# Performance work log

Hardware: AMD Instinct MI355X
Metric: run time of the kernel (lower is better)

## Reference

```python
import jax, jax.numpy as jnp
import numpy as np

N = 100000   # nodes
E = 1000000  # edges
D = 128      # hidden dim (all n_hidden entries)
ED = 21      # edge_dim hard-coded in the module


def setup_inputs() -> dict:
    key = jax.random.key(0)
    ks = jax.random.split(key, 32)
    w = lambda k, shape: (jax.random.normal(k, shape, dtype=jnp.float32) * 0.05)
    inp = {
        "G": jax.random.normal(ks[0], (N, D), dtype=jnp.float32),
        "edge_index": jax.random.randint(ks[1], (2, E), 0, N),
        "edge_attribute": jax.random.normal(ks[2], (E, ED), dtype=jnp.float32),
        # 3-layer node embedding MLP (stacked since all dims are D)
        "emb_W": w(ks[3], (3, D, D)), "emb_b": w(ks[4], (3, D)),
        # 2 ResGatedGraphConv layers (conv3 is unused in forward)
        "key_W": w(ks[5], (2, D, D)), "key_b": w(ks[6], (2, D)),
        "qry_W": w(ks[7], (2, D, D)), "qry_b": w(ks[8], (2, D)),
        "val_W": w(ks[9], (2, D, D)), "val_b": w(ks[10], (2, D)),
        "skp_W": w(ks[11], (2, D, D)), "skp_b": w(ks[12], (2, D)),
        "edg_W": w(ks[13], (2, ED, D)), "edg_b": w(ks[14], (2, D)),
        # graph linears
        "g1_W": w(ks[15], (D, D)), "g1_b": w(ks[16], (D,)),
        "g2_W": w(ks[17], (D, D)), "g2_b": w(ks[18], (D,)),
        # head: concat(node, graph_mean) -> 2D -> D -> D -> 1
        "h1_W": w(ks[19], (2 * D, D)), "h1_b": w(ks[20], (D,)),
        "h2_W": w(ks[21], (D, D)), "h2_b": w(ks[22], (D,)),
        "h3_W": w(ks[23], (D, 1)), "h3_b": w(ks[24], (1,)),
    }
    return inp


def reference(G, edge_index, edge_attribute,
              emb_W, emb_b, key_W, key_b, qry_W, qry_b, val_W, val_b,
              skp_W, skp_b, edg_W, edg_b,
              g1_W, g1_b, g2_W, g2_b, h1_W, h1_b, h2_W, h2_b, h3_W, h3_b):
    x = G
    # embedding MLP: Linear -> ReLU x3
    for i in range(3):
        x = jax.nn.relu(x @ emb_W[i] + emb_b[i])
    src, dst = edge_index[0], edge_index[1]
    # ResGatedGraphConv (PyG): out_i = W_skip x_i + sum_j sigmoid(k_i + q_j + W_e e_ij) * v_j
    for i in range(2):
        k = x @ key_W[i] + key_b[i]   # per target node i
        q = x @ qry_W[i] + qry_b[i]   # per source node j
        v = x @ val_W[i] + val_b[i]
        eta = jax.nn.sigmoid(k[dst] + q[src] + edge_attribute @ edg_W[i] + edg_b[i])  # [E, D]
        agg = jax.ops.segment_sum(eta * v[src], dst, num_segments=N)  # scatter-add [N, D]
        x = jax.nn.relu(agg + x @ skp_W[i] + skp_b[i])
    x = jax.nn.relu(x @ g1_W + g1_b)
    x = x @ g2_W + g2_b
    # per-node concat with mean-pooled graph embedding (vectorized form of the Python loop)
    gmean = jnp.mean(x, axis=0)
    u = jnp.concatenate([x, jnp.broadcast_to(gmean, x.shape)], axis=-1)  # [N, 2D]
    u = jax.nn.relu(u @ h1_W + h1_b)
    u = jax.nn.relu(u @ h2_W + h2_b)
    return u @ h3_W + h3_b  # [N, 1]
```

## Files before the change

### kernel.cpp

```cpp
#include <hip/hip_runtime.h>
#include <hip/hip_bf16.h>

#define DD 128
#define LW 136

typedef __attribute__((ext_vector_type(8))) short bf16x8;
typedef __attribute__((ext_vector_type(4))) float f32x4;

__device__ __forceinline__ void cvt8(const float4 a0, const float4 a1,
                                     bf16x8& hi, bf16x8& lo)
{
    float af[8] = {a0.x, a0.y, a0.z, a0.w, a1.x, a1.y, a1.z, a1.w};
    union { unsigned int u[4]; bf16x8 v; } H, L;
    #pragma unroll
    for (int i = 0; i < 4; ++i) {
        unsigned int b0 = __float_as_uint(af[2*i]);
        unsigned int b1 = __float_as_uint(af[2*i+1]);
        unsigned int h0 = b0 & 0xFFFF0000u;
        unsigned int h1 = b1 & 0xFFFF0000u;
        H.u[i] = (h0 >> 16) | h1;
        float r0 = af[2*i]   - __uint_as_float(h0);
        float r1 = af[2*i+1] - __uint_as_float(h1);
        L.u[i] = (__float_as_uint(r0) >> 16) | (__float_as_uint(r1) & 0xFFFF0000u);
    }
    hi = H.v; lo = L.v;
}

__device__ __forceinline__ float fsig(float z)
{
    return __builtin_amdgcn_rcpf(1.f + __expf(-z));
}

__device__ __forceinline__ void mfma_step(
    const unsigned short* __restrict__ WH, const unsigned short* __restrict__ WL,
    int wavecol, int l15, int kb,
    const bf16x8 ah[4], const bf16x8 al[4], f32x4 acc[4][2])
{
    bf16x8 bh[2], bl[2];
    #pragma unroll
    for (int ni = 0; ni < 2; ++ni) {
        int m = wavecol + ni * 16 + l15;
        bh[ni] = *(const bf16x8*)(WH + (size_t)m * DD + kb);
        bl[ni] = *(const bf16x8*)(WL + (size_t)m * DD + kb);
    }
    #pragma unroll
    for (int mi = 0; mi < 4; ++mi)
        #pragma unroll
        for (int ni = 0; ni < 2; ++ni) {
            acc[mi][ni] = __builtin_amdgcn_mfma_f32_16x16x32_bf16(ah[mi], bh[ni], acc[mi][ni], 0, 0, 0);
            acc[mi][ni] = __builtin_amdgcn_mfma_f32_16x16x32_bf16(ah[mi], bl[ni], acc[mi][ni], 0, 0, 0);
            acc[mi][ni] = __builtin_amdgcn_mfma_f32_16x16x32_bf16(al[mi], bh[ni], acc[mi][ni], 0, 0, 0);
        }
}

__device__ __forceinline__ void glb_layer(
    const float* __restrict__ X, int ldX, const int arow[4],
    const unsigned short* __restrict__ WU,
    int wavecol, int l15, int kg, f32x4 acc[4][2])
{
    const unsigned short* WH = WU;
    const unsigned short* WL = WU + 16384;
    #pragma unroll
    for (int kc = 0; kc < 4; ++kc) {
        const int kb = kc * 32 + kg;
        bf16x8 ah[4], al[4];
        #pragma unroll
        for (int mi = 0; mi < 4; ++mi) {
            const float* p = X + (size_t)arow[mi] * ldX + kb;
            float4 a0 = *(const float4*)p;
            float4 a1 = *(const float4*)(p + 4);
            cvt8(a0, a1, ah[mi], al[mi]);
        }
        mfma_step(WH, WL, wavecol, l15, kb, ah, al, acc);
    }
}

__device__ __forceinline__ void lds_layer(
    const unsigned short (*AH)[LW], const unsigned short (*AL)[LW],
    const unsigned short* __restrict__ WU,
    int wavecol, int l15, int kg, f32x4 acc[4][2])
{
    const unsigned short* WH = WU;
    const unsigned short* WL = WU + 16384;
    #pragma unroll
    for (int kc = 0; kc < 4; ++kc) {
        const int kb = kc * 32 + kg;
        bf16x8 ah[4], al[4];
        #pragma unroll
        for (int mi = 0; mi < 4; ++mi) {
            ah[mi] = *(const bf16x8*)&AH[mi * 16 + l15][kb];
            al[mi] = *(const bf16x8*)&AL[mi * 16 + l15][kb];
        }
        mfma_step(WH, WL, wavecol, l15, kb, ah, al, acc);
    }
}

__device__ __forceinline__ void epi_lds(
    const f32x4 acc[4][2], unsigned short (*AH)[LW], unsigned short (*AL)[LW],
    const float* __restrict__ bias, int wavecol, int l15, int rg, int relu)
{
    #pragma unroll
    for (int ni = 0; ni < 2; ++ni) {
        const int col = wavecol + ni * 16 + l15;
        const float bv = bias[col];
        #pragma unroll
        for (int mi = 0; mi < 4; ++mi)
            #pragma unroll
            for (int r = 0; r < 4; ++r) {
                const int row = mi * 16 + rg + r;
                float v = acc[mi][ni][r] + bv;
                if (relu) v = fmaxf(v, 0.f);
                unsigned int u = __float_as_uint(v), h = u & 0xFFFF0000u;
                float res = v - __uint_as_float(h);
                AH[row][col] = (unsigned short)(h >> 16);
                AL[row][col] = (unsigned short)(__float_as_uint(res) >> 16);
            }
    }
}

__global__ __launch_bounds__(256) void fused_emb3q(
    const float* __restrict__ G, const unsigned short* __restrict__ Wt,
    const float* __restrict__ embb, const float* __restrict__ biasCat,
    float* __restrict__ bfused, int N)
{
    __shared__ unsigned short AH[64][LW], AL[64][LW];
    const int lane = threadIdx.x & 63, wid = threadIdx.x >> 6;
    const int wavecol = wid * 32;
    const int l15 = lane & 15, kg = (lane >> 4) * 8, rg = (lane >> 4) * 4;
    const int row0 = blockIdx.x * 64;

    int arow[4];
    #pragma unroll
    for (int mi = 0; mi < 4; ++mi) {
        int r = row0 + mi * 16 + l15;
        arow[mi] = r < N ? r : N - 1;
    }

    f32x4 acc[4][2] = {};
    glb_layer(G, DD, arow, Wt, wavecol, l15, kg, acc);
    epi_lds(acc, AH, AL, embb, wavecol, l15, rg, 1);
    __syncthreads();

    #pragma unroll
    for (int mi = 0; mi < 4; ++mi)
        #pragma unroll
        for (int ni = 0; ni < 2; ++ni) acc[mi][ni] = (f32x4){0,0,0,0};
    lds_layer(AH, AL, Wt + 32768, wavecol, l15, kg, acc);
    __syncthreads();
    epi_lds(acc, AH, AL, embb + 128, wavecol, l15, rg, 1);
    __syncthreads();

    #pragma unroll
    for (int mi = 0; mi < 4; ++mi)
        #pragma unroll
        for (int ni = 0; ni < 2; ++ni) acc[mi][ni] = (f32x4){0,0,0,0};
    lds_layer(AH, AL, Wt + 65536, wavecol, l15, kg, acc);
    __syncthreads();
    epi_lds(acc, AH, AL, embb + 256, wavecol, l15, rg, 1);
    __syncthreads();

    for (int cb = 0; cb < 4; ++cb) {
        #pragma unroll
        for (int mi = 0; mi < 4; ++mi)
            #pragma unroll
            for (int ni = 0; ni < 2; ++ni) acc[mi][ni] = (f32x4){0,0,0,0};
        lds_layer(AH, AL, Wt + (size_t)(3 + cb) * 32768, wavecol, l15, kg, acc);
        #pragma unroll
        for (int ni = 0; ni < 2; ++ni) {
            const int gcol = cb * 128 + wavecol + ni * 16 + l15;
            const float bv = biasCat[gcol];
            #pragma unroll
            for (int mi = 0; mi < 4; ++mi)
                #pragma unroll
                for (int r = 0; r < 4; ++r) {
                    int row = row0 + mi * 16 + rg + r;
                    if (row < N)
                        bfused[(size_t)row * 512 + gcol] = acc[mi][ni][r] + bv;
                }
        }
    }
}

__global__ __launch_bounds__(256) void fused_kqvs(
    float* __restrict__ bfused, const unsigned short* __restrict__ Wt,
    const float* __restrict__ biasCat, int N)
{
    __shared__ unsigned short AH[64][LW], AL[64][LW];
    const int tid = threadIdx.x;
    const int lane = tid & 63, wid = tid >> 6;
    const int wavecol = wid * 32;
    const int l15 = lane & 15, kg = (lane >> 4) * 8, rg = (lane >> 4) * 4;
    const int row0 = blockIdx.x * 64;

    for (int idx = tid; idx < 64 * 128; idx += 256) {
        const int row = idx >> 7, col = idx & 127;
        int gr = row0 + row; if (gr >= N) gr = N - 1;
        float v = bfused[(size_t)gr * 512 + col];
        unsigned int u = __float_as_uint(v), h = u & 0xFFFF0000u;
        float res = v - __uint_as_float(h);
        AH[row][col] = (unsigned short)(h >> 16);
        AL[row][col] = (unsigned short)(__float_as_uint(res) >> 16);
    }
    __syncthreads();

    f32x4 acc[4][2];
    for (int cb = 0; cb < 4; ++cb) {
        #pragma unroll
        for (int mi = 0; mi < 4; ++mi)
            #pragma unroll
            for (int ni = 0; ni < 2; ++ni) acc[mi][ni] = (f32x4){0,0,0,0};
        lds_layer(AH, AL, Wt + (size_t)cb * 32768, wavecol, l15, kg, acc);
        #pragma unroll
        for (int ni = 0; ni < 2; ++ni) {
            const int gcol = cb * 128 + wavecol + ni * 16 + l15;
            const float bv = biasCat[cb * 128 + wavecol + ni * 16 + l15 - cb * 128 + cb * 128];
            #pragma unroll
            for (int mi = 0; mi < 4; ++mi)
                #pragma unroll
                for (int r = 0; r < 4; ++r) {
                    int row = row0 + mi * 16 + rg + r;
                    if (row < N)
                        bfused[(size_t)row * 512 + gcol] = acc[mi][ni][r] + bv;
                }
        }
    }
}

__global__ __launch_bounds__(256) void fused_g12(
    float* __restrict__ bfused, const unsigned short* __restrict__ Wt,
    const float* __restrict__ g1b, const float* __restrict__ g2b,
    float* __restrict__ gsum, int N)
{
    __shared__ unsigned short AH[64][LW], AL[64][LW];
    __shared__ float csum[128];
    const int tid = threadIdx.x;
    const int lane = tid & 63, wid = tid >> 6;
    const int wavecol = wid * 32;
    const int l15 = lane & 15, kg = (lane >> 4) * 8, rg = (lane >> 4) * 4;
    const int row0 = blockIdx.x * 64;

    if (tid < 128) csum[tid] = 0.f;

    int arow[4];
    #pragma unroll
    for (int mi = 0; mi < 4; ++mi) {
        int r = row0 + mi * 16 + l15;
        arow[mi] = r < N ? r : N - 1;
    }

    f32x4 acc[4][2] = {};
    glb_layer(bfused, 512, arow, Wt, wavecol, l15, kg, acc);
    epi_lds(acc, AH, AL, g1b, wavecol, l15, rg, 1);
    __syncthreads();

    #pragma unroll
    for (int mi = 0; mi < 4; ++mi)
        #pragma unroll
        for (int ni = 0; ni < 2; ++ni) acc[mi][ni] = (f32x4){0,0,0,0};
    lds_layer(AH, AL, Wt + 32768, wavecol, l15, kg, acc);

    #pragma unroll
    for (int ni = 0; ni < 2; ++ni) {
        const int col = wavecol + ni * 16 + l15;
        const float bv = g2b[col];
        float part = 0.f;
        #pragma unroll
        for (int mi = 0; mi < 4; ++mi)
            #pragma unroll
            for (int r = 0; r < 4; ++r) {
                int row = row0 + mi * 16 + rg + r;
                if (row < N) {
                    float v = acc[mi][ni][r] + bv;
                    bfused[(size_t)row * 512 + 128 + col] = v;
                    part += v;
                }
            }
        atomicAdd(&csum[col], part);
    }
    __syncthreads();
    if (tid < 128) atomicAdd(&gsum[tid], csum[tid]);
}

__global__ __launch_bounds__(256) void fused_head(
    const float* __restrict__ bfused, const unsigned short* __restrict__ Wt,
    const float* __restrict__ cvec, const float* __restrict__ h2b,
    const float* __restrict__ h3w, const float* __restrict__ h3b,
    float* __restrict__ out, int N)
{
    __shared__ unsigned short AH[64][LW], AL[64][LW];
    const int tid = threadIdx.x;
    const int lane = tid & 63, wid = tid >> 6;
    const int wavecol = wid * 32;
    const int l15 = lane & 15, kg = (lane >> 4) * 8, rg = (lane >> 4) * 4;
    const int row0 = blockIdx.x * 64;

    int arow[4];
    #pragma unroll
    for (int mi = 0; mi < 4; ++mi) {
        int r = row0 + mi * 16 + l15;
        arow[mi] = r < N ? r : N - 1;
    }

    f32x4 acc[4][2] = {};
    glb_layer(bfused + 128, 512, arow, Wt, wavecol, l15, kg, acc);
    epi_lds(acc, AH, AL, cvec, wavecol, l15, rg, 1);
    __syncthreads();

    #pragma unroll
    for (int mi = 0; mi < 4; ++mi)
        #pragma unroll
        for (int ni = 0; ni < 2; ++ni) acc[mi][ni] = (f32x4){0,0,0,0};
    lds_layer(AH, AL, Wt + 32768, wavecol, l15, kg, acc);
    __syncthreads();
    epi_lds(acc, AH, AL, h2b, wavecol, l15, rg, 1);
    __syncthreads();

    const int row = tid >> 2, seg = tid & 3;
    float s = 0.f;
    #pragma unroll 8
    for (int j = 0; j < 32; ++j) {
        int col = seg * 32 + j;
        float xv = __uint_as_float((unsigned int)AH[row][col] << 16)
                 + __uint_as_float((unsigned int)AL[row][col] << 16);
        s = fmaf(xv, h3w[col], s);
    }
    s += __shfl_xor(s, 1, 64);
    s += __shfl_xor(s, 2, 64);
    if (seg == 0 && row0 + row < N) out[row0 + row] = s + h3b[0];
}

__global__ __launch_bounds__(256) void prep_weights(
    const float* __restrict__ embW, const float* __restrict__ keyW,
    const float* __restrict__ qryW, const float* __restrict__ valW,
    const float* __restrict__ skpW, const float* __restrict__ g1W,
    const float* __restrict__ g2W, const float* __restrict__ h1W,
    const float* __restrict__ h2W,
    const float* __restrict__ keyb, const float* __restrict__ qryb,
    const float* __restrict__ valb, const float* __restrict__ skpb,
    unsigned short* __restrict__ Wt, float* __restrict__ biasCat)
{
    const int u = blockIdx.x;
    const int t = threadIdx.x;
    __shared__ float T[128][129];

    const float* src;
    if (u < 3)       src = embW + (size_t)u * 16384;
    else if (u < 7)  { const float* p[4] = {keyW, qryW, valW, skpW}; src = p[u - 3]; }
    else if (u < 11) { const float* p[4] = {keyW, qryW, valW, skpW}; src = p[u - 7] + 16384; }
    else if (u == 11) src = g1W;
    else if (u == 12) src = g2W;
    else if (u == 13) src = h1W;
    else              src = h2W;

    #pragma unroll
    for (int i = 0; i < 64; ++i) {
        int idx = t + 256 * i;
        T[idx >> 7][idx & 127] = src[idx];
    }
    __syncthreads();

    unsigned short* dH = Wt + (size_t)u * 32768;
    unsigned short* dL = dH + 16384;
    const int m = t >> 1, kbase = (t & 1) * 64;
    for (int j = 0; j < 64; ++j) {
        int k = kbase + j;
        float a = T[k][m];
        unsigned int b = __float_as_uint(a);
        unsigned int h = b & 0xFFFF0000u;
        float r = a - __uint_as_float(h);
        dH[m * 128 + k] = (unsigned short)(h >> 16);
        dL[m * 128 + k] = (unsigned short)(__float_as_uint(r) >> 16);
    }

    if (u == 0) {
        for (int x = t; x < 1024; x += 256) {
            int L = x >> 9, c = x & 511;
            const float* bp = (c < 128) ? keyb : (c < 256) ? qryb : (c < 384) ? valb : skpb;
            biasCat[x] = bp[L * 128 + (c & 127)];
        }
    }
}

__global__ void hist_kernel(const int* __restrict__ dstA, int* __restrict__ hist, int E)
{
    for (int e = blockIdx.x * blockDim.x + threadIdx.x; e < E;
         e += gridDim.x * blockDim.x)
        atomicAdd(&hist[dstA[e]], 1);
}

__global__ __launch_bounds__(256) void scan1_kernel(
    const int* __restrict__ in, int n_in,
    int* __restrict__ out, int* __restrict__ bsum, int n)
{
    __shared__ int wtot[4];
    const int t = threadIdx.x, lane = t & 63, wv = t >> 6;
    const int base = blockIdx.x * 1024 + t * 4;
    int v[4]; int sum = 0;
    #pragma unroll
    for (int j = 0; j < 4; ++j) {
        int idx = base + j;
        v[j] = (idx < n_in) ? in[idx] : 0;
        sum += v[j];
    }
    int incl = sum;
    #pragma unroll
    for (int d = 1; d < 64; d <<= 1) {
        int y = __shfl_up(incl, d, 64);
        if (lane >= d) incl += y;
    }
    if (lane == 63) wtot[wv] = incl;
    __syncthreads();
    int woff = 0;
    for (int w = 0; w < wv; ++w) woff += wtot[w];
    int run = woff + incl - sum;
    #pragma unroll
    for (int j = 0; j < 4; ++j) {
        int idx = base + j;
        if (idx < n) out[idx] = run;
        run += v[j];
    }
    if (t == 0)
        bsum[blockIdx.x] = wtot[0] + wtot[1] + wtot[2] + wtot[3];
}

__global__ void scan2_kernel(int* __restrict__ bsum, int nb)
{
    if (blockIdx.x == 0 && threadIdx.x == 0) {
        int run = 0;
        for (int i = 0; i < nb; ++i) { int t = bsum[i]; bsum[i] = run; run += t; }
    }
}

__global__ __launch_bounds__(256) void scan3_kernel(
    int* __restrict__ out, const int* __restrict__ bsum,
    int* __restrict__ cursor, int n, int n_nodes)
{
    const int base = blockIdx.x * 1024 + threadIdx.x * 4;
    const int add = bsum[blockIdx.x];
    #pragma unroll
    for (int j = 0; j < 4; ++j) {
        int idx = base + j;
        if (idx < n) {
            int vv = out[idx] + add;
            out[idx] = vv;
            if (idx < n_nodes) cursor[idx] = vv;
        }
    }
}

__global__ void scatter_kernel(const int* __restrict__ srcA, const int* __restrict__ dstA,
                               int* __restrict__ cursor, int* __restrict__ perm,
                               int* __restrict__ srcp, int E)
{
    for (int e = blockIdx.x * blockDim.x + threadIdx.x; e < E;
         e += gridDim.x * blockDim.x) {
        int d = dstA[e];
        int pos = atomicAdd(&cursor[d], 1);
        perm[pos] = e;
        srcp[pos] = srcA[e];
    }
}

__global__ void permute_ea_kernel(const float* __restrict__ ea, const int* __restrict__ perm,
                                  float* __restrict__ eaP, long E)
{
    const long total = E * 24;
    for (long t = (long)blockIdx.x * blockDim.x + threadIdx.x; t < total;
         t += (long)gridDim.x * blockDim.x) {
        long i = t / 24; int j = (int)(t - i * 24);
        eaP[t] = (j < 21) ? ea[(size_t)perm[i] * 21 + j] : 0.f;
    }
}

__global__ __launch_bounds__(256) void edge_agg13(
    const int* __restrict__ row_ptr, const int* __restrict__ srcp,
    const float* __restrict__ eaP,
    const float* __restrict__ We, const float* __restrict__ be,
    float* __restrict__ fused, int N)
{
    const int wv = threadIdx.x >> 6, lane = threadIdx.x & 63;
    const int d = blockIdx.x * 4 + wv;
    if (d >= N) return;
    const int c = lane * 2;

    float2 w[21];
    #pragma unroll
    for (int j = 0; j < 21; ++j)
        w[j] = *(const float2*)(We + j * DD + c);
    const float2 b2 = *(const float2*)(be + c);
    const float2 kd = *(const float2*)(fused + (size_t)d * 512 + c);
    const float2 sk = *(const float2*)(fused + (size_t)d * 512 + 384 + c);

    float ax = 0.f, ay = 0.f;
    const int i0 = __builtin_amdgcn_readfirstlane(row_ptr[d]);
    const int i1 = __builtin_amdgcn_readfirstlane(row_ptr[d + 1]);

    for (int i = i0; i < i1; i += 2) {
        const int iA = i;
        const int iB = (i + 1 < i1) ? i + 1 : i1 - 1;
        const float wgtB = (i + 1 < i1) ? 1.f : 0.f;

        const int sA = __builtin_amdgcn_readfirstlane(srcp[iA]);
        const int sB = __builtin_amdgcn_readfirstlane(srcp[iB]);

        const float* eA = eaP + (size_t)iA * 24;
        const float* eB = eaP + (size_t)iB * 24;
        float aA[21], aB[21];
        #pragma unroll
        for (int j = 0; j < 21; ++j) { aA[j] = eA[j]; aB[j] = eB[j]; }

        const float* fpA = fused + (size_t)sA * 512;
        const float* fpB = fused + (size_t)sB * 512;
        float2 qA = *(const float2*)(fpA + 128 + c);
        float2 vA = *(const float2*)(fpA + 256 + c);
        float2 qB = *(const float2*)(fpB + 128 + c);
        float2 vB = *(const float2*)(fpB + 256 + c);

        float pxA[4] = {0,0,0,0}, pyA[4] = {0,0,0,0};
        float pxB[4] = {0,0,0,0}, pyB[4] = {0,0,0,0};
        #pragma unroll
        for (int j = 0; j < 21; ++j) {
            int s = j & 3;
            pxA[s] = fmaf(aA[j], w[j].x, pxA[s]);
            pyA[s] = fmaf(aA[j], w[j].y, pyA[s]);
            pxB[s] = fmaf(aB[j], w[j].x, pxB[s]);
            pyB[s] = fmaf(aB[j], w[j].y, pyB[s]);
        }
        float exA = (pxA[0] + pxA[1]) + (pxA[2] + pxA[3]) + b2.x;
        float eyA = (pyA[0] + pyA[1]) + (pyA[2] + pyA[3]) + b2.y;
        float exB = (pxB[0] + pxB[1]) + (pxB[2] + pxB[3]) + b2.x;
        float eyB = (pyB[0] + pyB[1]) + (pyB[2] + pyB[3]) + b2.y;

        float gxA = fsig(kd.x + qA.x + exA);
        float gyA = fsig(kd.y + qA.y + eyA);
        float gxB = wgtB * fsig(kd.x + qB.x + exB);
        float gyB = wgtB * fsig(kd.y + qB.y + eyB);

        ax = fmaf(gxA, vA.x, ax);
        ay = fmaf(gyA, vA.y, ay);
        ax = fmaf(gxB, vB.x, ax);
        ay = fmaf(gyB, vB.y, ay);
    }

    float* xr = fused + (size_t)d * 512;
    xr[c]     = fmaxf(ax + sk.x, 0.f);
    xr[c + 1] = fmaxf(ay + sk.y, 0.f);
}

__global__ void cvec_kernel(const float* __restrict__ gsum, const float* __restrict__ h1W,
                            const float* __restrict__ h1b, float* __restrict__ cvec, float invN)
{
    const int m = threadIdx.x;
    float acc = h1b[m];
    for (int k = 0; k < 128; ++k)
        acc = fmaf(gsum[k] * invN, h1W[(size_t)(128 + k) * DD + m], acc);
    cvec[m] = acc;
}

extern "C" void kernel_launch(void* const* d_in, const int* in_sizes, int n_in,
                              void* d_out, int out_size, void* d_ws, size_t ws_size,
                              hipStream_t stream)
{
    const float* G    = (const float*)d_in[0];
    const int*   ei   = (const int*)  d_in[1];
    const float* ea   = (const float*)d_in[2];
    const float* embW = (const float*)d_in[3];
    const float* embb = (const float*)d_in[4];
    const float* keyW = (const float*)d_in[5];
    const float* keyb = (const float*)d_in[6];
    const float* qryW = (const float*)d_in[7];
    const float* qryb = (const float*)d_in[8];
    const float* valW = (const float*)d_in[9];
    const float* valb = (const float*)d_in[10];
    const float* skpW = (const float*)d_in[11];
    const float* skpb = (const float*)d_in[12];
    const float* edgW = (const float*)d_in[13];
    const float* edgb = (const float*)d_in[14];
    const float* g1W  = (const float*)d_in[15];
    const float* g1b  = (const float*)d_in[16];
    const float* g2W  = (const float*)d_in[17];
    const float* g2b  = (const float*)d_in[18];
    const float* h1W  = (const float*)d_in[19];
    const float* h1b  = (const float*)d_in[20];
    const float* h2W  = (const float*)d_in[21];
    const float* h2b  = (const float*)d_in[22];
    const float* h3W  = (const float*)d_in[23];
    const float* h3b  = (const float*)d_in[24];

    const int N = in_sizes[0] / DD;
    const int E = in_sizes[2] / 21;
    const int* srcA = ei;
    const int* dstA = ei + E;

    float* bfused = (float*)d_ws;
    float* gsum   = bfused + (size_t)N * 512;
    float* cvec   = gsum + DD;
    float* biasCat= cvec + DD;
    unsigned short* Wt = (unsigned short*)(biasCat + 1024);
    int* hist = (int*)((char*)Wt + (size_t)15 * 32768 * 2);
    int* row  = hist + N;
    int* cur  = row + N + 1;
    int* bsum = cur + N;
    int* perm = bsum + 128;
    int* srcp = perm + E;
    float* eaP = (float*)(srcp + E);

    const int fgrid   = (N + 63) / 64;
    const int aggGrid = (N + 3) / 4;
    const int nScan = N + 1;
    const int nb = (nScan + 1023) / 1024;

    prep_weights<<<15, 256, 0, stream>>>(embW, keyW, qryW, valW, skpW,
                                         g1W, g2W, h1W, h2W,
                                         keyb, qryb, valb, skpb, Wt, biasCat);
    hipMemsetAsync(hist, 0, (size_t)N * sizeof(int), stream);
    hipMemsetAsync(gsum, 0, DD * sizeof(float), stream);
    hist_kernel<<<1024, 256, 0, stream>>>(dstA, hist, E);
    scan1_kernel<<<nb, 256, 0, stream>>>(hist, N, row, bsum, nScan);
    scan2_kernel<<<1, 64, 0, stream>>>(bsum, nb);
    scan3_kernel<<<nb, 256, 0, stream>>>(row, bsum, cur, nScan, N);
    scatter_kernel<<<1024, 256, 0, stream>>>(srcA, dstA, cur, perm, srcp, E);
    permute_ea_kernel<<<2048, 256, 0, stream>>>(ea, perm, eaP, (long)E);

    #define UNIT(u) (Wt + (size_t)(u) * 32768)

    fused_emb3q<<<fgrid, 256, 0, stream>>>(G, Wt, embb, biasCat, bfused, N);

    edge_agg13<<<aggGrid, 256, 0, stream>>>(row, srcp, eaP,
                                            edgW + 0, edgb + 0, bfused, N);

    fused_kqvs<<<fgrid, 256, 0, stream>>>(bfused, UNIT(7), biasCat + 512, N);
    edge_agg13<<<aggGrid, 256, 0, stream>>>(row, srcp, eaP,
                                            edgW + 21*DD, edgb + DD, bfused, N);

    fused_g12<<<fgrid, 256, 0, stream>>>(bfused, UNIT(11), g1b, g2b, gsum, N);

    cvec_kernel<<<1, DD, 0, stream>>>(gsum, h1W, h1b, cvec, 1.0f / (float)N);

    fused_head<<<fgrid, 256, 0, stream>>>(bfused, UNIT(13), cvec, h2b, h3W, h3b,
                                          (float*)d_out, N);
}
```

Before: 1.093 ms.

## Fuse edge-attribute permutation into scatter and prefetch next gather in edge aggregation

The CSR scatter kernel now copies each edge's 21 attributes directly into the permuted padded buffer, which removes the separate perm array and the permute_ea kernel. The edge aggregation kernel software-pipelines the q/v gathers by loading the next pair of source rows while the current pair is computed. The intent is to cut one pass over the edge attributes and hide gather latency. In exchange, the scatter writes are strided per thread (less coalesced) and the loop uses more registers. The pad columns of eaP are no longer zeroed, but they are never read.

```diff
diff --git a/kernel.cpp b/kernel.cpp
--- a/kernel.cpp
+++ b/kernel.cpp
@@ -213,7 +213,7 @@
         #pragma unroll
         for (int ni = 0; ni < 2; ++ni) {
             const int gcol = cb * 128 + wavecol + ni * 16 + l15;
-            const float bv = biasCat[cb * 128 + wavecol + ni * 16 + l15 - cb * 128 + cb * 128];
+            const float bv = biasCat[gcol];
             #pragma unroll
             for (int mi = 0; mi < 4; ++mi)
                 #pragma unroll
@@ -448,31 +448,23 @@
     }
 }
 
-__global__ void scatter_kernel(const int* __restrict__ srcA, const int* __restrict__ dstA,
-                               int* __restrict__ cursor, int* __restrict__ perm,
-                               int* __restrict__ srcp, int E)
+__global__ void scatter_ea(const int* __restrict__ srcA, const int* __restrict__ dstA,
+                           const float* __restrict__ ea, int* __restrict__ cursor,
+                           int* __restrict__ srcp, float* __restrict__ eaP, int E)
 {
     for (int e = blockIdx.x * blockDim.x + threadIdx.x; e < E;
          e += gridDim.x * blockDim.x) {
         int d = dstA[e];
         int pos = atomicAdd(&cursor[d], 1);
-        perm[pos] = e;
         srcp[pos] = srcA[e];
-    }
-}
-
-__global__ void permute_ea_kernel(const float* __restrict__ ea, const int* __restrict__ perm,
-                                  float* __restrict__ eaP, long E)
-{
-    const long total = E * 24;
-    for (long t = (long)blockIdx.x * blockDim.x + threadIdx.x; t < total;
-         t += (long)gridDim.x * blockDim.x) {
-        long i = t / 24; int j = (int)(t - i * 24);
-        eaP[t] = (j < 21) ? ea[(size_t)perm[i] * 21 + j] : 0.f;
-    }
-}
-
-__global__ __launch_bounds__(256) void edge_agg13(
+        const float* s = ea + (size_t)e * 21;
+        float* q = eaP + (size_t)pos * 24;
+        #pragma unroll
+        for (int j = 0; j < 21; ++j) q[j] = s[j];
+    }
+}
+
+__global__ __launch_bounds__(256) void edge_agg14(
     const int* __restrict__ row_ptr, const int* __restrict__ srcp,
     const float* __restrict__ eaP,
     const float* __restrict__ We, const float* __restrict__ be,
@@ -495,26 +487,43 @@
     const int i0 = __builtin_amdgcn_readfirstlane(row_ptr[d]);
     const int i1 = __builtin_amdgcn_readfirstlane(row_ptr[d + 1]);
 
-    for (int i = i0; i < i1; i += 2) {
-        const int iA = i;
-        const int iB = (i + 1 < i1) ? i + 1 : i1 - 1;
-        const float wgtB = (i + 1 < i1) ? 1.f : 0.f;
-
-        const int sA = __builtin_amdgcn_readfirstlane(srcp[iA]);
-        const int sB = __builtin_amdgcn_readfirstlane(srcp[iB]);
-
-        const float* eA = eaP + (size_t)iA * 24;
-        const float* eB = eaP + (size_t)iB * 24;
-        float aA[21], aB[21];
-        #pragma unroll
-        for (int j = 0; j < 21; ++j) { aA[j] = eA[j]; aB[j] = eB[j]; }
-
+    float2 qA = {0,0}, vA = {0,0}, qB = {0,0}, vB = {0,0};
+    if (i0 < i1) {
+        const int iB0 = (i0 + 1 < i1) ? i0 + 1 : i0;
+        const int sA = __builtin_amdgcn_readfirstlane(srcp[i0]);
+        const int sB = __builtin_amdgcn_readfirstlane(srcp[iB0]);
         const float* fpA = fused + (size_t)sA * 512;
         const float* fpB = fused + (size_t)sB * 512;
-        float2 qA = *(const float2*)(fpA + 128 + c);
-        float2 vA = *(const float2*)(fpA + 256 + c);
-        float2 qB = *(const float2*)(fpB + 128 + c);
-        float2 vB = *(const float2*)(fpB + 256 + c);
+        qA = *(const float2*)(fpA + 128 + c);
+        vA = *(const float2*)(fpA + 256 + c);
+        qB = *(const float2*)(fpB + 128 + c);
+        vB = *(const float2*)(fpB + 256 + c);
+    }
+
+    for (int i = i0; i < i1; i += 2) {
+        const float wgtB = (i + 1 < i1) ? 1.f : 0.f;
+        const int iBc = (i + 1 < i1) ? i + 1 : i;
+
+        const float2 cqA = qA, cvA = vA, cqB = qB, cvB = vB;
+
+        const int inx = i + 2;
+        if (inx < i1) {
+            const int inB = (inx + 1 < i1) ? inx + 1 : inx;
+            const int sA = __builtin_amdgcn_readfirstlane(srcp[inx]);
+            const int sB = __builtin_amdgcn_readfirstlane(srcp[inB]);
+            const float* fpA = fused + (size_t)sA * 512;
+            const float* fpB = fused + (size_t)sB * 512;
+            qA = *(const float2*)(fpA + 128 + c);
+            vA = *(const float2*)(fpA + 256 + c);
+            qB = *(const float2*)(fpB + 128 + c);
+            vB = *(const float2*)(fpB + 256 + c);
+        }
+
+        const float* eA = eaP + (size_t)i * 24;
+        const float* eB = eaP + (size_t)iBc * 24;
+        float aA[21], aB[21];
+        #pragma unroll
+        for (int j = 0; j < 21; ++j) { aA[j] = eA[j]; aB[j] = eB[j]; }
 
         float pxA[4] = {0,0,0,0}, pyA[4] = {0,0,0,0};
         float pxB[4] = {0,0,0,0}, pyB[4] = {0,0,0,0};
@@ -531,15 +540,15 @@
         float exB = (pxB[0] + pxB[1]) + (pxB[2] + pxB[3]) + b2.x;
         float eyB = (pyB[0] + pyB[1]) + (pyB[2] + pyB[3]) + b2.y;
 
-        float gxA = fsig(kd.x + qA.x + exA);
-        float gyA = fsig(kd.y + qA.y + eyA);
-        float gxB = wgtB * fsig(kd.x + qB.x + exB);
-        float gyB = wgtB * fsig(kd.y + qB.y + eyB);
-
-        ax = fmaf(gxA, vA.x, ax);
-        ay = fmaf(gyA, vA.y, ay);
-        ax = fmaf(gxB, vB.x, ax);
-        ay = fmaf(gyB, vB.y, ay);
+        float gxA = fsig(kd.x + cqA.x + exA);
+        float gyA = fsig(kd.y + cqA.y + eyA);
+        float gxB = wgtB * fsig(kd.x + cqB.x + exB);
+        float gyB = wgtB * fsig(kd.y + cqB.y + eyB);
+
+        ax = fmaf(gxA, cvA.x, ax);
+        ay = fmaf(gyA, cvA.y, ay);
+        ax = fmaf(gxB, cvB.x, ax);
+        ay = fmaf(gyB, cvB.y, ay);
     }
 
     float* xr = fused + (size_t)d * 512;
@@ -601,8 +610,7 @@
     int* row  = hist + N;
     int* cur  = row + N + 1;
     int* bsum = cur + N;
-    int* perm = bsum + 128;
-    int* srcp = perm + E;
+    int* srcp = bsum + 128;
     float* eaP = (float*)(srcp + E);
 
     const int fgrid   = (N + 63) / 64;
@@ -619,18 +627,17 @@
     scan1_kernel<<<nb, 256, 0, stream>>>(hist, N, row, bsum, nScan);
     scan2_kernel<<<1, 64, 0, stream>>>(bsum, nb);
     scan3_kernel<<<nb, 256, 0, stream>>>(row, bsum, cur, nScan, N);
-    scatter_kernel<<<1024, 256, 0, stream>>>(srcA, dstA, cur, perm, srcp, E);
-    permute_ea_kernel<<<2048, 256, 0, stream>>>(ea, perm, eaP, (long)E);
+    scatter_ea<<<1024, 256, 0, stream>>>(srcA, dstA, ea, cur, srcp, eaP, E);
 
     #define UNIT(u) (Wt + (size_t)(u) * 32768)
 
     fused_emb3q<<<fgrid, 256, 0, stream>>>(G, Wt, embb, biasCat, bfused, N);
 
-    edge_agg13<<<aggGrid, 256, 0, stream>>>(row, srcp, eaP,
+    edge_agg14<<<aggGrid, 256, 0, stream>>>(row, srcp, eaP,
                                             edgW + 0, edgb + 0, bfused, N);
 
     fused_kqvs<<<fgrid, 256, 0, stream>>>(bfused, UNIT(7), biasCat + 512, N);
-    edge_agg13<<<aggGrid, 256, 0, stream>>>(row, srcp, eaP,
+    edge_agg14<<<aggGrid, 256, 0, stream>>>(row, srcp, eaP,
                                             edgW + 21*DD, edgb + DD, bfused, N);
 
     fused_g12<<<fgrid, 256, 0, stream>>>(bfused, UNIT(11), g1b, g2b, gsum, N);
```

Result: faster. 1.028 ms (median of 2 runs) (-5.9%).

## Fuse edge-attribute permutation into CSR scatter and persist edge aggregation grid

Applied to the files above, without the earlier changes.

The CSR scatter kernel now copies each edge's 21 attributes straight to their sorted slot. This removes the separate perm array and the permute_ea pass with its per-element index divide. The edge aggregation kernel becomes a grid-stride loop over destination nodes with a fixed 2048-block grid, so the 21 edge weights are loaded once per wave instead of once per node. The trade-offs are fewer waves to hide gather latency, uncoalesced 21-float writes in the scatter, and the 3 padding floats in eaP no longer being written (they are unread).

```diff
diff --git a/kernel.cpp b/kernel.cpp
--- a/kernel.cpp
+++ b/kernel.cpp
@@ -213,7 +213,7 @@
         #pragma unroll
         for (int ni = 0; ni < 2; ++ni) {
             const int gcol = cb * 128 + wavecol + ni * 16 + l15;
-            const float bv = biasCat[cb * 128 + wavecol + ni * 16 + l15 - cb * 128 + cb * 128];
+            const float bv = biasCat[gcol];
             #pragma unroll
             for (int mi = 0; mi < 4; ++mi)
                 #pragma unroll
@@ -448,39 +448,29 @@
     }
 }
 
-__global__ void scatter_kernel(const int* __restrict__ srcA, const int* __restrict__ dstA,
-                               int* __restrict__ cursor, int* __restrict__ perm,
-                               int* __restrict__ srcp, int E)
+__global__ void scatter_ea(const int* __restrict__ srcA, const int* __restrict__ dstA,
+                           const float* __restrict__ ea, int* __restrict__ cursor,
+                           int* __restrict__ srcp, float* __restrict__ eaP, int E)
 {
     for (int e = blockIdx.x * blockDim.x + threadIdx.x; e < E;
          e += gridDim.x * blockDim.x) {
         int d = dstA[e];
         int pos = atomicAdd(&cursor[d], 1);
-        perm[pos] = e;
         srcp[pos] = srcA[e];
-    }
-}
-
-__global__ void permute_ea_kernel(const float* __restrict__ ea, const int* __restrict__ perm,
-                                  float* __restrict__ eaP, long E)
-{
-    const long total = E * 24;
-    for (long t = (long)blockIdx.x * blockDim.x + threadIdx.x; t < total;
-         t += (long)gridDim.x * blockDim.x) {
-        long i = t / 24; int j = (int)(t - i * 24);
-        eaP[t] = (j < 21) ? ea[(size_t)perm[i] * 21 + j] : 0.f;
-    }
-}
-
-__global__ __launch_bounds__(256) void edge_agg13(
+        const float* s = ea + (size_t)e * 21;
+        float* q = eaP + (size_t)pos * 24;
+        #pragma unroll
+        for (int j = 0; j < 21; ++j) q[j] = s[j];
+    }
+}
+
+__global__ __launch_bounds__(256) void edge_agg16(
     const int* __restrict__ row_ptr, const int* __restrict__ srcp,
     const float* __restrict__ eaP,
     const float* __restrict__ We, const float* __restrict__ be,
     float* __restrict__ fused, int N)
 {
     const int wv = threadIdx.x >> 6, lane = threadIdx.x & 63;
-    const int d = blockIdx.x * 4 + wv;
-    if (d >= N) return;
     const int c = lane * 2;
 
     float2 w[21];
@@ -488,63 +478,68 @@
     for (int j = 0; j < 21; ++j)
         w[j] = *(const float2*)(We + j * DD + c);
     const float2 b2 = *(const float2*)(be + c);
-    const float2 kd = *(const float2*)(fused + (size_t)d * 512 + c);
-    const float2 sk = *(const float2*)(fused + (size_t)d * 512 + 384 + c);
-
-    float ax = 0.f, ay = 0.f;
-    const int i0 = __builtin_amdgcn_readfirstlane(row_ptr[d]);
-    const int i1 = __builtin_amdgcn_readfirstlane(row_ptr[d + 1]);
-
-    for (int i = i0; i < i1; i += 2) {
-        const int iA = i;
-        const int iB = (i + 1 < i1) ? i + 1 : i1 - 1;
-        const float wgtB = (i + 1 < i1) ? 1.f : 0.f;
-
-        const int sA = __builtin_amdgcn_readfirstlane(srcp[iA]);
-        const int sB = __builtin_amdgcn_readfirstlane(srcp[iB]);
-
-        const float* eA = eaP + (size_t)iA * 24;
-        const float* eB = eaP + (size_t)iB * 24;
-        float aA[21], aB[21];
-        #pragma unroll
-        for (int j = 0; j < 21; ++j) { aA[j] = eA[j]; aB[j] = eB[j]; }
-
-        const float* fpA = fused + (size_t)sA * 512;
-        const float* fpB = fused + (size_t)sB * 512;
-        float2 qA = *(const float2*)(fpA + 128 + c);
-        float2 vA = *(const float2*)(fpA + 256 + c);
-        float2 qB = *(const float2*)(fpB + 128 + c);
-        float2 vB = *(const float2*)(fpB + 256 + c);
-
-        float pxA[4] = {0,0,0,0}, pyA[4] = {0,0,0,0};
-        float pxB[4] = {0,0,0,0}, pyB[4] = {0,0,0,0};
-        #pragma unroll
-        for (int j = 0; j < 21; ++j) {
-            int s = j & 3;
-            pxA[s] = fmaf(aA[j], w[j].x, pxA[s]);
-            pyA[s] = fmaf(aA[j], w[j].y, pyA[s]);
-            pxB[s] = fmaf(aB[j], w[j].x, pxB[s]);
-            pyB[s] = fmaf(aB[j], w[j].y, pyB[s]);
-        }
-        float exA = (pxA[0] + pxA[1]) + (pxA[2] + pxA[3]) + b2.x;
-        float eyA = (pyA[0] + pyA[1]) + (pyA[2] + pyA[3]) + b2.y;
-        float exB = (pxB[0] + pxB[1]) + (pxB[2] + pxB[3]) + b2.x;
-        float eyB = (pyB[0] + pyB[1]) + (pyB[2] + pyB[3]) + b2.y;
-
-        float gxA = fsig(kd.x + qA.x + exA);
-        float gyA = fsig(kd.y + qA.y + eyA);
-        float gxB = wgtB * fsig(kd.x + qB.x + exB);
-        float gyB = wgtB * fsig(kd.y + qB.y + eyB);
-
-        ax = fmaf(gxA, vA.x, ax);
-        ay = fmaf(gyA, vA.y, ay);
-        ax = fmaf(gxB, vB.x, ax);
-        ay = fmaf(gyB, vB.y, ay);
-    }
-
-    float* xr = fused + (size_t)d * 512;
-    xr[c]     = fmaxf(ax + sk.x, 0.f);
-    xr[c + 1] = fmaxf(ay + sk.y, 0.f);
+
+    const int dstride = gridDim.x * 4;
+
+    for (int d = blockIdx.x * 4 + wv; d < N; d += dstride) {
+        const float2 kd = *(const float2*)(fused + (size_t)d * 512 + c);
+        const float2 sk = *(const float2*)(fused + (size_t)d * 512 + 384 + c);
+
+        float ax = 0.f, ay = 0.f;
+        const int i0 = __builtin_amdgcn_readfirstlane(row_ptr[d]);
+        const int i1 = __builtin_amdgcn_readfirstlane(row_ptr[d + 1]);
+
+        for (int i = i0; i < i1; i += 2) {
+            const int iA = i;
+            const int iB = (i + 1 < i1) ? i + 1 : i1 - 1;
+            const float wgtB = (i + 1 < i1) ? 1.f : 0.f;
+
+            const int sA = __builtin_amdgcn_readfirstlane(srcp[iA]);
+            const int sB = __builtin_amdgcn_readfirstlane(srcp[iB]);
+
+            const float* eA = eaP + (size_t)iA * 24;
+            const float* eB = eaP + (size_t)iB * 24;
+            float aA[21], aB[21];
+            #pragma unroll
+            for (int j = 0; j < 21; ++j) { aA[j] = eA[j]; aB[j] = eB[j]; }
+
+            const float* fpA = fused + (size_t)sA * 512;
+            const float* fpB = fused + (size_t)sB * 512;
+            float2 qA = *(const float2*)(fpA + 128 + c);
+            float2 vA = *(const float2*)(fpA + 256 + c);
+            float2 qB = *(const float2*)(fpB + 128 + c);
+            float2 vB = *(const float2*)(fpB + 256 + c);
+
+            float pxA[4] = {0,0,0,0}, pyA[4] = {0,0,0,0};
+            float pxB[4] = {0,0,0,0}, pyB[4] = {0,0,0,0};
+            #pragma unroll
+            for (int j = 0; j < 21; ++j) {
+                int s = j & 3;
+                pxA[s] = fmaf(aA[j], w[j].x, pxA[s]);
+                pyA[s] = fmaf(aA[j], w[j].y, pyA[s]);
+                pxB[s] = fmaf(aB[j], w[j].x, pxB[s]);
+                pyB[s] = fmaf(aB[j], w[j].y, pyB[s]);
+            }
+            float exA = (pxA[0] + pxA[1]) + (pxA[2] + pxA[3]) + b2.x;
+            float eyA = (pyA[0] + pyA[1]) + (pyA[2] + pyA[3]) + b2.y;
+            float exB = (pxB[0] + pxB[1]) + (pxB[2] + pxB[3]) + b2.x;
+            float eyB = (pyB[0] + pyB[1]) + (pyB[2] + pyB[3]) + b2.y;
+
+            float gxA = fsig(kd.x + qA.x + exA);
+            float gyA = fsig(kd.y + qA.y + eyA);
+            float gxB = wgtB * fsig(kd.x + qB.x + exB);
+            float gyB = wgtB * fsig(kd.y + qB.y + eyB);
+
+            ax = fmaf(gxA, vA.x, ax);
+            ay = fmaf(gyA, vA.y, ay);
+            ax = fmaf(gxB, vB.x, ax);
+            ay = fmaf(gyB, vB.y, ay);
+        }
+
+        float* xr = fused + (size_t)d * 512;
+        xr[c]     = fmaxf(ax + sk.x, 0.f);
+        xr[c + 1] = fmaxf(ay + sk.y, 0.f);
+    }
 }
 
 __global__ void cvec_kernel(const float* __restrict__ gsum, const float* __restrict__ h1W,
@@ -601,12 +596,11 @@
     int* row  = hist + N;
     int* cur  = row + N + 1;
     int* bsum = cur + N;
-    int* perm = bsum + 128;
-    int* srcp = perm + E;
+    int* srcp = bsum + 128;
     float* eaP = (float*)(srcp + E);
 
     const int fgrid   = (N + 63) / 64;
-    const int aggGrid = (N + 3) / 4;
+    const int aggGrid = 2048;
     const int nScan = N + 1;
     const int nb = (nScan + 1023) / 1024;
 
@@ -619,18 +613,17 @@
     scan1_kernel<<<nb, 256, 0, stream>>>(hist, N, row, bsum, nScan);
     scan2_kernel<<<1, 64, 0, stream>>>(bsum, nb);
     scan3_kernel<<<nb, 256, 0, stream>>>(row, bsum, cur, nScan, N);
-    scatter_kernel<<<1024, 256, 0, stream>>>(srcA, dstA, cur, perm, srcp, E);
-    permute_ea_kernel<<<2048, 256, 0, stream>>>(ea, perm, eaP, (long)E);
+    scatter_ea<<<1024, 256, 0, stream>>>(srcA, dstA, ea, cur, srcp, eaP, E);
 
     #define UNIT(u) (Wt + (size_t)(u) * 32768)
 
     fused_emb3q<<<fgrid, 256, 0, stream>>>(G, Wt, embb, biasCat, bfused, N);
 
-    edge_agg13<<<aggGrid, 256, 0, stream>>>(row, srcp, eaP,
+    edge_agg16<<<aggGrid, 256, 0, stream>>>(row, srcp, eaP,
                                             edgW + 0, edgb + 0, bfused, N);
 
     fused_kqvs<<<fgrid, 256, 0, stream>>>(bfused, UNIT(7), biasCat + 512, N);
-    edge_agg13<<<aggGrid, 256, 0, stream>>>(row, srcp, eaP,
+    edge_agg16<<<aggGrid, 256, 0, stream>>>(row, srcp, eaP,
                                             edgW + 21*DD, edgb + DD, bfused, N);
 
     fused_g12<<<fgrid, 256, 0, stream>>>(bfused, UNIT(11), g1b, g2b, gsum, N);
```

New measurement: 1.077 ms. Within noise of the previous version (-1.5%).
